# Kernel tuning notes

Measured on AMD Instinct MI355X. Metric: run time of the kernel, lower is better.

The kernel has to match this reference:

```python
import jax, jax.numpy as jnp
import numpy as np

B = 8        # segments (batch elements)
NPER = 512   # blocks per segment
U = 4        # units per block (fixed, unit2block = repeat(arange(N), U))
N = B * NPER # total blocks
K = 16


def setup_inputs() -> dict:
    key = jax.random.key(0)
    unit_pos = jax.random.normal(key, (N * U, 3), dtype=jnp.float32) * 10.0
    base = jnp.arange(N, dtype=jnp.int32).reshape(B, NPER)
    # all intra-segment pairs: row repeated, col tiled, per segment
    row = jnp.repeat(base, NPER, axis=1).reshape(-1)          # [E]
    col = jnp.tile(base, (1, NPER)).reshape(-1)               # [E]
    unit2block = jnp.repeat(jnp.arange(N, dtype=jnp.int32), U)
    segment_ids = jnp.repeat(jnp.arange(B, dtype=jnp.int32), NPER)
    return dict(unit_pos=unit_pos, row=row, col=col,
                unit2block=unit2block, segment_ids=segment_ids, k=K)


def reference(unit_pos, row, col, unit2block, segment_ids, k):
    # pre_filter: scope='both' and min_dist=0 -> keep all candidate edges.
    n_blocks = unit_pos.shape[0] // U
    pos = unit_pos.reshape(n_blocks, U, 3)  # units grouped by block (unit2block is sorted)
    pi = pos[row]  # [E,U,3]
    pj = pos[col]  # [E,U,3]
    # block-block distance = min pairwise unit distance (||a-b||^2 via expansion)
    d2 = (jnp.sum(pi * pi, -1)[:, :, None]
          + jnp.sum(pj * pj, -1)[:, None, :]
          - 2.0 * jnp.einsum('eud,evd->euv', pi, pj))            # [E,U,U]
    dist = jnp.min(jnp.sqrt(jnp.maximum(d2, 0.0)), axis=(1, 2))  # [E]
    # scatter_topk(dist, row, k, largest=False): sort by dist, stable-sort by row,
    # keep first k entries per row segment. Every row has exactly C candidates.
    order = jnp.argsort(dist)                                   # ascending dist
    perm = order[jnp.argsort(row[order], stable=True)]          # grouped by row, dist-ascending within
    C = row.shape[0] // n_blocks                                # candidates per row (uniform)
    sel = perm.reshape(n_blocks, C)[:, :k].reshape(-1)          # [N*k] original edge indices
    row_o = row[sel]
    col_o = col[sel]
    attr = jnp.zeros_like(row_o)
    return row_o, col_o, attr
```

## Files before the change

kernel.cpp:

```cpp
#include <hip/hip_runtime.h>

namespace {
constexpr int NPER = 512;
constexpr int UU   = 4;
constexpr int KK   = 16;
constexpr int NB   = 4096;
constexpr int STRIDE = 13;
constexpr int NK = NB * KK;

template <int CTRL, int RM>
__device__ __forceinline__ void dpp_min_step(unsigned& lo, unsigned& hi) {
    unsigned lo2 = (unsigned)__builtin_amdgcn_update_dpp(
        (int)0xFFFFFFFF, (int)lo, CTRL, RM, 0xF, false);
    unsigned hi2 = (unsigned)__builtin_amdgcn_update_dpp(
        (int)0xFFFFFFFF, (int)hi, CTRL, RM, 0xF, false);
    unsigned long long a = ((unsigned long long)hi << 32) | lo;
    unsigned long long b = ((unsigned long long)hi2 << 32) | lo2;
    if (b < a) { lo = lo2; hi = hi2; }
}

__device__ __forceinline__ unsigned long long wave_min_u64(unsigned long long v) {
    unsigned lo = (unsigned)v, hi = (unsigned)(v >> 32);
    dpp_min_step<0x111, 0xF>(lo, hi);
    dpp_min_step<0x112, 0xF>(lo, hi);
    dpp_min_step<0x114, 0xF>(lo, hi);
    dpp_min_step<0x118, 0xF>(lo, hi);
    dpp_min_step<0x142, 0xA>(lo, hi);
    dpp_min_step<0x143, 0xC>(lo, hi);
    unsigned mlo = (unsigned)__builtin_amdgcn_readlane((int)lo, 63);
    unsigned mhi = (unsigned)__builtin_amdgcn_readlane((int)hi, 63);
    return ((unsigned long long)mhi << 32) | mlo;
}

__global__ __launch_bounds__(256) void knn_edge_kernel(const float* __restrict__ unit_pos,
                                                       int* __restrict__ out) {
    __shared__ float sp[NPER * STRIDE];
    const int wg  = blockIdx.x;
    const int seg = (wg * 4) >> 9;
    const int tid = threadIdx.x;

    const float4* g4 = reinterpret_cast<const float4*>(
        unit_pos + (size_t)seg * NPER * UU * 3);
    #pragma unroll
    for (int j = 0; j < 6; ++j) {
        const int i = tid + 256 * j;
        const float4 v = g4[i];
        const int c = i / 3;
        const int part = (i - 3 * c) * 4;
        float* d = &sp[c * STRIDE + part];
        d[0] = v.x; d[1] = v.y; d[2] = v.z; d[3] = v.w;
    }
    __syncthreads();

    const int wave = tid >> 6;
    const int lane = tid & 63;
    const int r_local  = (wg * 4 + wave) & (NPER - 1);
    const int r_global = seg * NPER + r_local;

    float xi[UU], yi[UU], zi[UU], ai[UU];
    #pragma unroll
    for (int u = 0; u < UU; ++u) {
        const float* p = &sp[r_local * STRIDE + u * 3];
        xi[u] = p[0]; yi[u] = p[1]; zi[u] = p[2];
        ai[u] = __fadd_rn(__fadd_rn(__fmul_rn(xi[u], xi[u]),
                                    __fmul_rn(yi[u], yi[u])),
                          __fmul_rn(zi[u], zi[u]));
    }

    unsigned long long key[8];
    #pragma unroll
    for (int t = 0; t < 8; ++t) {
        const int c = lane + 64 * t;
        const float* p = &sp[c * STRIDE];
        float xj[UU], yj[UU], zj[UU], aj[UU];
        #pragma unroll
        for (int v = 0; v < UU; ++v) {
            xj[v] = p[v * 3 + 0]; yj[v] = p[v * 3 + 1]; zj[v] = p[v * 3 + 2];
            aj[v] = __fadd_rn(__fadd_rn(__fmul_rn(xj[v], xj[v]),
                                        __fmul_rn(yj[v], yj[v])),
                              __fmul_rn(zj[v], zj[v]));
        }
        float m = __builtin_inff();
        #pragma unroll
        for (int u = 0; u < UU; ++u) {
            #pragma unroll
            for (int v = 0; v < UU; ++v) {
                float dot = __fadd_rn(__fadd_rn(__fmul_rn(xi[u], xj[v]),
                                                __fmul_rn(yi[u], yj[v])),
                                      __fmul_rn(zi[u], zj[v]));
                float d2 = __fsub_rn(__fadd_rn(ai[u], aj[v]), __fmul_rn(2.0f, dot));
                d2 = fmaxf(d2, 0.0f);
                m  = fminf(m, d2);
            }
        }
        float dist = __fsqrt_rn(m);
        key[t] = ((unsigned long long)__float_as_uint(dist) << 32) | (unsigned int)c;
    }

    int mycol = 0;
    #pragma unroll
    for (int it = 0; it < KK; ++it) {
        unsigned long long lm = key[0];
        #pragma unroll
        for (int t = 1; t < 8; ++t) lm = key[t] < lm ? key[t] : lm;
        const unsigned long long m = wave_min_u64(lm);
        if (lane == it) mycol = (int)(unsigned)(m & 0xffffffffull);
        #pragma unroll
        for (int t = 0; t < 8; ++t)
            if (key[t] == m) key[t] = 0xffffffffffffffffull;
    }

    if (lane < KK) {
        const int o = r_global * KK + lane;
        out[o]          = r_global;
        out[NK + o]     = (seg * NPER) + mycol;
        out[2 * NK + o] = 0;
    }
}
}

extern "C" void kernel_launch(void* const* d_in, const int* in_sizes, int n_in,
                              void* d_out, int out_size, void* d_ws, size_t ws_size,
                              hipStream_t stream) {
    const float* unit_pos = (const float*)d_in[0];
    int* out = (int*)d_out;
    hipLaunchKernelGGL(knn_edge_kernel, dim3(NB / 4), dim3(256), 0, stream,
                       unit_pos, out);
}
```

Before: 25.38 us.

## Split each row's candidates across two waves and merge top-k via shared-memory rank

Each row's 512 candidates are now split between two waves of a 512-thread block. Each wave finds its own 16 smallest keys, and the two lists are merged by rank counting over 32 keys in shared memory. Shared memory now uses an unpadded stride of 12 floats, filled by direct float4 copies and read with float4 loads. This halves the serial top-16 extraction chain per wave and raises the wave count, at the cost of an extra block barrier, a merge step, and possible LDS bank conflicts from the unpadded stride.

```diff
diff --git a/kernel.cpp b/kernel.cpp
--- a/kernel.cpp
+++ b/kernel.cpp
@@ -5,8 +5,8 @@
 constexpr int UU   = 4;
 constexpr int KK   = 16;
 constexpr int NB   = 4096;
-constexpr int STRIDE = 13;
-constexpr int NK = NB * KK;
+constexpr int NK   = NB * KK;
+constexpr int SFL  = 12;
 
 template <int CTRL, int RM>
 __device__ __forceinline__ void dpp_min_step(unsigned& lo, unsigned& hi) {
@@ -32,63 +32,69 @@
     return ((unsigned long long)mhi << 32) | mlo;
 }
 
-__global__ __launch_bounds__(256) void knn_edge_kernel(const float* __restrict__ unit_pos,
-                                                       int* __restrict__ out) {
-    __shared__ float sp[NPER * STRIDE];
+__global__ __launch_bounds__(512, 8) void knn_edge_kernel(const float* __restrict__ unit_pos,
+                                                          int* __restrict__ out) {
+    __shared__ float sp[NPER * SFL];
+    __shared__ unsigned long long mb[4][2 * KK];
+
     const int wg  = blockIdx.x;
     const int seg = (wg * 4) >> 9;
     const int tid = threadIdx.x;
 
-    const float4* g4 = reinterpret_cast<const float4*>(
-        unit_pos + (size_t)seg * NPER * UU * 3);
-    #pragma unroll
-    for (int j = 0; j < 6; ++j) {
-        const int i = tid + 256 * j;
-        const float4 v = g4[i];
-        const int c = i / 3;
-        const int part = (i - 3 * c) * 4;
-        float* d = &sp[c * STRIDE + part];
-        d[0] = v.x; d[1] = v.y; d[2] = v.z; d[3] = v.w;
+    {
+        const float4* g4 = reinterpret_cast<const float4*>(
+            unit_pos + (size_t)seg * NPER * UU * 3);
+        float4* s4 = reinterpret_cast<float4*>(sp);
+        #pragma unroll
+        for (int j = 0; j < 3; ++j) s4[tid + 512 * j] = g4[tid + 512 * j];
     }
     __syncthreads();
 
     const int wave = tid >> 6;
     const int lane = tid & 63;
-    const int r_local  = (wg * 4 + wave) & (NPER - 1);
-    const int r_global = seg * NPER + r_local;
+    const int row_local = (wg * 4 + (wave >> 1)) & (NPER - 1);
+    const int half = wave & 1;
 
     float xi[UU], yi[UU], zi[UU], ai[UU];
-    #pragma unroll
-    for (int u = 0; u < UU; ++u) {
-        const float* p = &sp[r_local * STRIDE + u * 3];
-        xi[u] = p[0]; yi[u] = p[1]; zi[u] = p[2];
-        ai[u] = __fadd_rn(__fadd_rn(__fmul_rn(xi[u], xi[u]),
-                                    __fmul_rn(yi[u], yi[u])),
-                          __fmul_rn(zi[u], zi[u]));
+    {
+        const float4 r0 = *reinterpret_cast<const float4*>(&sp[row_local * SFL + 0]);
+        const float4 r1 = *reinterpret_cast<const float4*>(&sp[row_local * SFL + 4]);
+        const float4 r2 = *reinterpret_cast<const float4*>(&sp[row_local * SFL + 8]);
+        xi[0] = r0.x; yi[0] = r0.y; zi[0] = r0.z;
+        xi[1] = r0.w; yi[1] = r1.x; zi[1] = r1.y;
+        xi[2] = r1.z; yi[2] = r1.w; zi[2] = r2.x;
+        xi[3] = r2.y; yi[3] = r2.z; zi[3] = r2.w;
+        #pragma unroll
+        for (int u = 0; u < UU; ++u)
+            ai[u] = __fadd_rn(__fadd_rn(__fmul_rn(xi[u], xi[u]),
+                                        __fmul_rn(yi[u], yi[u])),
+                              __fmul_rn(zi[u], zi[u]));
     }
 
-    unsigned long long key[8];
+    unsigned long long key[4];
     #pragma unroll
-    for (int t = 0; t < 8; ++t) {
-        const int c = lane + 64 * t;
-        const float* p = &sp[c * STRIDE];
-        float xj[UU], yj[UU], zj[UU], aj[UU];
+    for (int t = 0; t < 4; ++t) {
+        const int c = half * 256 + lane + 64 * t;
+        const float4 q0 = *reinterpret_cast<const float4*>(&sp[c * SFL + 0]);
+        const float4 q1 = *reinterpret_cast<const float4*>(&sp[c * SFL + 4]);
+        const float4 q2 = *reinterpret_cast<const float4*>(&sp[c * SFL + 8]);
+        float xj[UU], yj[UU], zj[UU];
+        xj[0] = q0.x; yj[0] = q0.y; zj[0] = q0.z;
+        xj[1] = q0.w; yj[1] = q1.x; zj[1] = q1.y;
+        xj[2] = q1.z; yj[2] = q1.w; zj[2] = q2.x;
+        xj[3] = q2.y; yj[3] = q2.z; zj[3] = q2.w;
+        float m = __builtin_inff();
         #pragma unroll
         for (int v = 0; v < UU; ++v) {
-            xj[v] = p[v * 3 + 0]; yj[v] = p[v * 3 + 1]; zj[v] = p[v * 3 + 2];
-            aj[v] = __fadd_rn(__fadd_rn(__fmul_rn(xj[v], xj[v]),
-                                        __fmul_rn(yj[v], yj[v])),
-                              __fmul_rn(zj[v], zj[v]));
-        }
-        float m = __builtin_inff();
-        #pragma unroll
-        for (int u = 0; u < UU; ++u) {
+            const float aj = __fadd_rn(__fadd_rn(__fmul_rn(xj[v], xj[v]),
+                                                 __fmul_rn(yj[v], yj[v])),
+                                       __fmul_rn(zj[v], zj[v]));
             #pragma unroll
-            for (int v = 0; v < UU; ++v) {
+            for (int u = 0; u < UU; ++u) {
                 float dot = __fadd_rn(__fadd_rn(__fmul_rn(xi[u], xj[v]),
                                                 __fmul_rn(yi[u], yj[v])),
                                       __fmul_rn(zi[u], zj[v]));
-                float d2 = __fsub_rn(__fadd_rn(ai[u], aj[v]), __fmul_rn(2.0f, dot));
+                float d2 = __fsub_rn(__fadd_rn(ai[u], aj), __fmul_rn(2.0f, dot));
                 d2 = fmaxf(d2, 0.0f);
                 m  = fminf(m, d2);
             }
@@ -97,24 +103,39 @@
         key[t] = ((unsigned long long)__float_as_uint(dist) << 32) | (unsigned int)c;
     }
 
-    int mycol = 0;
+    unsigned long long mykey = 0xFFFFFFFFFFFFFFFFull;
     #pragma unroll
     for (int it = 0; it < KK; ++it) {
         unsigned long long lm = key[0];
         #pragma unroll
-        for (int t = 1; t < 8; ++t) lm = key[t] < lm ? key[t] : lm;
+        for (int t = 1; t < 4; ++t) lm = key[t] < lm ? key[t] : lm;
         const unsigned long long m = wave_min_u64(lm);
-        if (lane == it) mycol = (int)(unsigned)(m & 0xffffffffull);
+        if (lane == it) mykey = m;
         #pragma unroll
-        for (int t = 0; t < 8; ++t)
-            if (key[t] == m) key[t] = 0xffffffffffffffffull;
+        for (int t = 0; t < 4; ++t)
+            if (key[t] == m) key[t] = 0xFFFFFFFFFFFFFFFFull;
     }
+    if (lane < KK) mb[wave >> 1][half * KK + lane] = mykey;
+    __syncthreads();
 
-    if (lane < KK) {
-        const int o = r_global * KK + lane;
-        out[o]          = r_global;
-        out[NK + o]     = (seg * NPER) + mycol;
-        out[2 * NK + o] = 0;
+    if (wave < 4) {
+        const int r_global = seg * NPER + ((wg * 4 + wave) & (NPER - 1));
+        if (lane < 2 * KK) {
+            const unsigned long long k = mb[wave][lane];
+            int rank = 0;
+            #pragma unroll 8
+            for (int m = 0; m < 2 * KK; ++m)
+                rank += (mb[wave][m] < k) ? 1 : 0;
+            if (rank < KK) {
+                const int c = (int)(unsigned)(k & 0xFFFFFFFFull);
+                out[NK + r_global * KK + rank] = seg * NPER + c;
+            }
+        }
+        if (lane < KK) {
+            const int o = r_global * KK + lane;
+            out[o]          = r_global;
+            out[2 * NK + o] = 0;
+        }
     }
 }
 }
@@ -124,6 +145,6 @@
                               hipStream_t stream) {
     const float* unit_pos = (const float*)d_in[0];
     int* out = (int*)d_out;
-    hipLaunchKernelGGL(knn_edge_kernel, dim3(NB / 4), dim3(256), 0, stream,
+    hipLaunchKernelGGL(knn_edge_kernel, dim3(NB / 4), dim3(512), 0, stream,
                        unit_pos, out);
 }
```

Measured after the change: 100.4 us. 296% more time.

## Use packed f32 math with SoA shared layout for distance computation

Applied to the files above, without the earlier changes.

Changes the shared-memory layout to a structure-of-arrays per block (x0..x3, y0..y3, z0..z3) padded to 9 doubles so each column can be read with 64-bit loads. The 16 pairwise unit distances are computed with v_pk_mul/add/fma_f32 inline asm, processing two units per instruction, which halves the VALU instruction count of the inner loop. Clamping to zero is moved after the min. The final expression uses an FMA with -2, so rounding may differ slightly from the reference's separate multiply and subtract, and tie ordering could change.

```diff
diff --git a/kernel.cpp b/kernel.cpp
--- a/kernel.cpp
+++ b/kernel.cpp
@@ -5,8 +5,23 @@
 constexpr int UU   = 4;
 constexpr int KK   = 16;
 constexpr int NB   = 4096;
-constexpr int STRIDE = 13;
-constexpr int NK = NB * KK;
+constexpr int NK   = NB * KK;
+constexpr int DST  = 9;
+
+union pk2 { double d; float f[2]; unsigned u[2]; };
+
+__device__ __forceinline__ double mkpk(float lo, float hi) {
+    pk2 t; t.f[0] = lo; t.f[1] = hi; return t.d;
+}
+__device__ __forceinline__ double pk_mul(double a, double b) {
+    double r; asm("v_pk_mul_f32 %0, %1, %2" : "=v"(r) : "v"(a), "v"(b)); return r;
+}
+__device__ __forceinline__ double pk_add(double a, double b) {
+    double r; asm("v_pk_add_f32 %0, %1, %2" : "=v"(r) : "v"(a), "v"(b)); return r;
+}
+__device__ __forceinline__ double pk_fma(double a, double b, double c) {
+    double r; asm("v_pk_fma_f32 %0, %1, %2, %3" : "=v"(r) : "v"(a), "v"(b), "v"(c)); return r;
+}
 
 template <int CTRL, int RM>
 __device__ __forceinline__ void dpp_min_step(unsigned& lo, unsigned& hi) {
@@ -18,7 +33,6 @@
     unsigned long long b = ((unsigned long long)hi2 << 32) | lo2;
     if (b < a) { lo = lo2; hi = hi2; }
 }
-
 __device__ __forceinline__ unsigned long long wave_min_u64(unsigned long long v) {
     unsigned lo = (unsigned)v, hi = (unsigned)(v >> 32);
     dpp_min_step<0x111, 0xF>(lo, hi);
@@ -34,21 +48,29 @@
 
 __global__ __launch_bounds__(256) void knn_edge_kernel(const float* __restrict__ unit_pos,
                                                        int* __restrict__ out) {
-    __shared__ float sp[NPER * STRIDE];
+    __shared__ double spd[NPER * DST];
+    float* sfl = reinterpret_cast<float*>(spd);
+
     const int wg  = blockIdx.x;
     const int seg = (wg * 4) >> 9;
     const int tid = threadIdx.x;
 
-    const float4* g4 = reinterpret_cast<const float4*>(
-        unit_pos + (size_t)seg * NPER * UU * 3);
-    #pragma unroll
-    for (int j = 0; j < 6; ++j) {
-        const int i = tid + 256 * j;
-        const float4 v = g4[i];
-        const int c = i / 3;
-        const int part = (i - 3 * c) * 4;
-        float* d = &sp[c * STRIDE + part];
-        d[0] = v.x; d[1] = v.y; d[2] = v.z; d[3] = v.w;
+    {
+        const float4* g4 = reinterpret_cast<const float4*>(
+            unit_pos + (size_t)seg * NPER * UU * 3);
+        #pragma unroll
+        for (int jj = 0; jj < 6; ++jj) {
+            const int i4 = tid + 256 * jj;
+            const float4 v = g4[i4];
+            const int c = i4 / 3;
+            const int rem = (i4 - 3 * c) * 4;
+            const float vv[4] = {v.x, v.y, v.z, v.w};
+            #pragma unroll
+            for (int e = 0; e < 4; ++e) {
+                const int j = rem + e, u = j / 3, ax = j - 3 * u;
+                sfl[c * (2 * DST) + ax * 4 + u] = vv[e];
+            }
+        }
     }
     __syncthreads();
 
@@ -57,44 +79,56 @@
     const int r_local  = (wg * 4 + wave) & (NPER - 1);
     const int r_global = seg * NPER + r_local;
 
-    float xi[UU], yi[UU], zi[UU], ai[UU];
-    #pragma unroll
-    for (int u = 0; u < UU; ++u) {
-        const float* p = &sp[r_local * STRIDE + u * 3];
-        xi[u] = p[0]; yi[u] = p[1]; zi[u] = p[2];
-        ai[u] = __fadd_rn(__fadd_rn(__fmul_rn(xi[u], xi[u]),
-                                    __fmul_rn(yi[u], yi[u])),
-                          __fmul_rn(zi[u], zi[u]));
+    double xi_p[UU], yi_p[UU], zi_p[UU], ai_p[UU];
+    {
+        const float* rp = &sfl[r_local * (2 * DST)];
+        #pragma unroll
+        for (int u = 0; u < UU; ++u) {
+            const float x = rp[0 * 4 + u], y = rp[1 * 4 + u], z = rp[2 * 4 + u];
+            const float a = __fadd_rn(__fadd_rn(__fmul_rn(x, x), __fmul_rn(y, y)),
+                                      __fmul_rn(z, z));
+            xi_p[u] = mkpk(x, x); yi_p[u] = mkpk(y, y);
+            zi_p[u] = mkpk(z, z); ai_p[u] = mkpk(a, a);
+        }
     }
+    const double m2 = mkpk(-2.0f, -2.0f);
 
     unsigned long long key[8];
     #pragma unroll
     for (int t = 0; t < 8; ++t) {
         const int c = lane + 64 * t;
-        const float* p = &sp[c * STRIDE];
-        float xj[UU], yj[UU], zj[UU], aj[UU];
-        #pragma unroll
-        for (int v = 0; v < UU; ++v) {
-            xj[v] = p[v * 3 + 0]; yj[v] = p[v * 3 + 1]; zj[v] = p[v * 3 + 2];
-            aj[v] = __fadd_rn(__fadd_rn(__fmul_rn(xj[v], xj[v]),
-                                        __fmul_rn(yj[v], yj[v])),
-                              __fmul_rn(zj[v], zj[v]));
-        }
-        float m = __builtin_inff();
+        const double* cp = &spd[c * DST];
+        const double x01 = cp[0], x23 = cp[1];
+        const double y01 = cp[2], y23 = cp[3];
+        const double z01 = cp[4], z23 = cp[5];
+        const double aj01 = pk_add(pk_add(pk_mul(x01, x01), pk_mul(y01, y01)),
+                                   pk_mul(z01, z01));
+        const double aj23 = pk_add(pk_add(pk_mul(x23, x23), pk_mul(y23, y23)),
+                                   pk_mul(z23, z23));
+        pk2 h[8];
         #pragma unroll
         for (int u = 0; u < UU; ++u) {
-            #pragma unroll
-            for (int v = 0; v < UU; ++v) {
-                float dot = __fadd_rn(__fadd_rn(__fmul_rn(xi[u], xj[v]),
-                                                __fmul_rn(yi[u], yj[v])),
-                                      __fmul_rn(zi[u], zj[v]));
-                float d2 = __fsub_rn(__fadd_rn(ai[u], aj[v]), __fmul_rn(2.0f, dot));
-                d2 = fmaxf(d2, 0.0f);
-                m  = fminf(m, d2);
-            }
+            const double dot01 = pk_add(pk_add(pk_mul(xi_p[u], x01),
+                                               pk_mul(yi_p[u], y01)),
+                                        pk_mul(zi_p[u], z01));
+            const double dot23 = pk_add(pk_add(pk_mul(xi_p[u], x23),
+                                               pk_mul(yi_p[u], y23)),
+                                        pk_mul(zi_p[u], z23));
+            h[u].d     = pk_fma(dot01, m2, pk_add(ai_p[u], aj01));
+            h[4 + u].d = pk_fma(dot23, m2, pk_add(ai_p[u], aj23));
         }
-        float dist = __fsqrt_rn(m);
-        key[t] = ((unsigned long long)__float_as_uint(dist) << 32) | (unsigned int)c;
+        const float m01 = fminf(fminf(h[0].f[0], h[0].f[1]),
+                                fminf(h[1].f[0], h[1].f[1]));
+        const float m23 = fminf(fminf(h[2].f[0], h[2].f[1]),
+                                fminf(h[3].f[0], h[3].f[1]));
+        const float m45 = fminf(fminf(h[4].f[0], h[4].f[1]),
+                                fminf(h[5].f[0], h[5].f[1]));
+        const float m67 = fminf(fminf(h[6].f[0], h[6].f[1]),
+                                fminf(h[7].f[0], h[7].f[1]));
+        float m = fminf(fminf(m01, m23), fminf(m45, m67));
+        m = fmaxf(m, 0.0f);
+        const float dist = __fsqrt_rn(m);
+        key[t] = ((unsigned long long)__float_as_uint(dist) << 32) | (unsigned)c;
     }
 
     int mycol = 0;
@@ -107,7 +141,7 @@
         if (lane == it) mycol = (int)(unsigned)(m & 0xffffffffull);
         #pragma unroll
         for (int t = 0; t < 8; ++t)
-            if (key[t] == m) key[t] = 0xffffffffffffffffull;
+            if (key[t] == m) key[t] = 0xFFFFFFFFFFFFFFFFull;
     }
 
     if (lane < KK) {
```

After: 24.00 us. -5.5%, faster.
